# Optimization experiments

Measured on AMD Instinct MI355X. Metric: run time of the kernel, lower is better.

## Reference

```python
import jax, jax.numpy as jnp
import numpy as np

N_NODES = 65536
N_EDGES = 1048576
IN_F = 128
HID_F = 128
OUT_F = 128


def setup_inputs() -> dict:
    key = jax.random.key(0)
    ks = jax.random.split(key, 8)
    feat = jax.random.normal(ks[0], (N_NODES, IN_F), dtype=jnp.float32)
    eweight = jax.random.uniform(ks[1], (N_EDGES, 1), dtype=jnp.float32)
    W1 = jax.random.normal(ks[2], (IN_F, HID_F), dtype=jnp.float32) * (1.0 / np.sqrt(IN_F))
    b1 = jnp.zeros((HID_F,), dtype=jnp.float32)
    W2 = jax.random.normal(ks[3], (HID_F, OUT_F), dtype=jnp.float32) * (1.0 / np.sqrt(HID_F))
    b2 = jnp.zeros((OUT_F,), dtype=jnp.float32)
    src = jax.random.randint(ks[4], (N_EDGES,), 0, N_NODES, dtype=jnp.int32)
    dst = jax.random.randint(ks[5], (N_EDGES,), 0, N_NODES, dtype=jnp.int32)
    return {"feat": feat, "eweight": eweight, "W1": W1, "b1": b1,
            "W2": W2, "b2": b2, "src": src, "dst": dst}


def _degrees(src, dst, n_nodes):
    ones = jnp.ones(src.shape[0], dtype=jnp.float32)
    deg_out = jax.ops.segment_sum(ones, src, num_segments=n_nodes)
    deg_in = jax.ops.segment_sum(ones, dst, num_segments=n_nodes)
    # DGL GraphConv clamps degree to min 1 before norm='both'
    return jnp.clip(deg_out, 1.0, None), jnp.clip(deg_in, 1.0, None)


def _graph_conv(feat, W, b, src, dst, out_norm, in_norm, n_nodes):
    # DGL GraphConv, norm='both': D_out^{-1/2} x -> x W -> spmm sum -> D_in^{-1/2} -> + b
    h = feat * out_norm[:, None]
    h = h @ W
    agg = jax.ops.segment_sum(h[src], dst, num_segments=n_nodes)
    return agg * in_norm[:, None] + b


def reference(feat, eweight, W1, b1, W2, b2, src, dst):
    n = feat.shape[0]
    deg_out, deg_in = _degrees(src, dst, n)
    out_norm = jax.lax.rsqrt(deg_out)
    in_norm = jax.lax.rsqrt(deg_in)
    h = _graph_conv(feat, W1, b1, src, dst, out_norm, in_norm, n)
    h = jax.nn.relu(h)
    h = _graph_conv(h, W2, b2, src, dst, out_norm, in_norm, n)
    # final update_all: u_mul_e + sum (eweight given)
    msg = h[src] * eweight  # [E, OUT_F]
    return jax.ops.segment_sum(msg, dst, num_segments=n)
```

## Files before the change

kernel.cpp:

```cpp
#include <hip/hip_runtime.h>

#define F 128
#define NBA 512
#define NBS 128
#define COARSE 256
#define CAP_BIN 4864
#define CAP_CSR 5632

typedef unsigned int uint;
typedef unsigned short ushort;
typedef unsigned char uchar;
typedef __attribute__((ext_vector_type(8))) short short8;
typedef __attribute__((ext_vector_type(8))) unsigned short ushort8;
typedef __attribute__((ext_vector_type(4))) float floatx4;

__device__ __forceinline__ ushort f2bf(float f) {
  uint u = __float_as_uint(f);
  u += 0x7fffu + ((u >> 16) & 1u);
  return (ushort)(u >> 16);
}

__global__ __launch_bounds__(256) void w_prep(const float* __restrict__ W1,
                                              const float* __restrict__ W2,
                                              ushort* __restrict__ W1t,
                                              ushort* __restrict__ W2t,
                                              int* __restrict__ cursorD,
                                              int* __restrict__ cursorS) {
  int b = blockIdx.x;
  if (b == 0) cursorD[threadIdx.x] = 0;
  if (b == 1) cursorS[threadIdx.x] = 0;
  const float* W = (b < 64) ? W1 : W2;
  ushort* Wt = (b < 64) ? W1t : W2t;
  int idx = (b & 63) * 256 + threadIdx.x;
  int k = idx >> 7, n = idx & 127;
  Wt[n * F + k] = f2bf(W[idx]);
}

__global__ __launch_bounds__(256) void bin_edges(
    const int* __restrict__ src, const int* __restrict__ dst,
    const float* __restrict__ ew, int E,
    int* __restrict__ cursorD, int* __restrict__ cursorS,
    uint2* __restrict__ slotD, uchar* __restrict__ srcF) {
  __shared__ int cnt[4][COARSE];
  __shared__ int base[COARSE];
  bool isD = blockIdx.x < NBA;
  int blk = isD ? blockIdx.x : blockIdx.x - NBA;
  int nblk = isD ? NBA : NBS;
  const int* key = isD ? dst : src;
  int* cursor = isD ? cursorD : cursorS;
  int wave = threadIdx.x >> 6;
  for (int i = threadIdx.x; i < 4 * COARSE; i += 256) ((int*)cnt)[i] = 0;
  __syncthreads();
  int chunk = (E + nblk - 1) / nblk;
  int s0 = blk * chunk, s1 = min(E, s0 + chunk);
  for (int i = s0 + threadIdx.x; i < s1; i += 256)
    atomicAdd(&cnt[wave][key[i] >> 8], 1);
  __syncthreads();
  if (threadIdx.x < COARSE) {
    int b = threadIdx.x;
    int tot = cnt[0][b] + cnt[1][b] + cnt[2][b] + cnt[3][b];
    base[b] = tot ? atomicAdd(&cursor[b], tot) : 0;
    cnt[0][b] = 0;
  }
  __syncthreads();
  if (isD) {
    for (int i = s0 + threadIdx.x; i < s1; i += 256) {
      int d = dst[i];
      int bin = d >> 8;
      int p = base[bin] + atomicAdd(&cnt[0][bin], 1);
      if (p < CAP_BIN) {
        uint2 v;
        v.x = (uint)(src[i] & 0xffff) | ((uint)f2bf(ew[i]) << 16);
        v.y = (uint)(d & 255);
        slotD[(size_t)bin * CAP_BIN + p] = v;
      }
    }
  } else {
    for (int i = s0 + threadIdx.x; i < s1; i += 256) {
      int s = src[i];
      int bin = s >> 8;
      int p = base[bin] + atomicAdd(&cnt[0][bin], 1);
      if (p < CAP_BIN) srcF[(size_t)bin * CAP_BIN + p] = (uchar)(s & 255);
    }
  }
}

__global__ __launch_bounds__(1024) void bucket_csr(
    const uint2* __restrict__ slotD, const int* __restrict__ cursorD,
    int2* __restrict__ rowRange, float* __restrict__ inNorm, uint* __restrict__ csr,
    const uchar* __restrict__ srcF, const int* __restrict__ cursorS,
    float* __restrict__ outNorm) {
  __shared__ int hist[256], base[256], cur[256];
  int t = threadIdx.x;
  if (blockIdx.x >= COARSE) {
    int b = blockIdx.x - COARSE;
    int lo = b * CAP_BIN;
    int cntS = min(cursorS[b], CAP_BIN);
    if (t < 256) hist[t] = 0;
    __syncthreads();
    for (int i = lo + t; i < lo + cntS; i += 1024)
      atomicAdd(&hist[srcF[i]], 1);
    __syncthreads();
    if (t < 256) outNorm[b * 256 + t] = rsqrtf((float)max(hist[t], 1));
    return;
  }
  int b = blockIdx.x;
  int lo = b * CAP_BIN;
  int cntD = min(cursorD[b], CAP_BIN);
  int hi = lo + cntD;
  if (t < 256) hist[t] = 0;
  __syncthreads();
  for (int i = lo + t; i < hi; i += 1024)
    atomicAdd(&hist[slotD[i].y], 1);
  __syncthreads();
  if (t < 256) base[t] = (hist[t] + 3) & ~3;
  __syncthreads();
  for (int off = 1; off < 256; off <<= 1) {
    int x = 0;
    if (t < 256 && t >= off) x = base[t - off];
    __syncthreads();
    if (t < 256) base[t] += x;
    __syncthreads();
  }
  if (t < 256) {
    int v = hist[t];
    int sz4 = (v + 3) & ~3;
    int st = b * CAP_CSR + base[t] - sz4;
    base[t] = st;
    cur[t] = 0;
    int node = b * 256 + t;
    rowRange[node] = make_int2(st, v);
    inNorm[node] = rsqrtf((float)max(v, 1));
  }
  __syncthreads();
  for (int i = lo + t; i < hi; i += 1024) {
    uint2 v = slotD[i];
    int fine = v.y;
    int p = base[fine] + atomicAdd(&cur[fine], 1);
    csr[p] = v.x;
  }
}

template <bool BF16IN>
__global__ __launch_bounds__(256) void gemm_mfma(
    const void* __restrict__ Xv, const float* __restrict__ scale,
    const ushort* __restrict__ Wt, ushort* __restrict__ Y) {
  __shared__ ushort sA[128 * 136];
  __shared__ ushort sB[128 * 136];
  int t = threadIdx.x;
  int row0 = blockIdx.x * 128;

  {
    int r = t >> 1, hf = t & 1;
    ushort* ap = sA + r * 136 + hf * 64;
    if (BF16IN) {
      const ushort* xp = (const ushort*)Xv + (size_t)(row0 + r) * F + hf * 64;
#pragma unroll
      for (int j = 0; j < 8; ++j)
        *(ushort8*)(ap + j * 8) = *(const ushort8*)(xp + j * 8);
    } else {
      const float* xp = (const float*)Xv + (size_t)(row0 + r) * F + hf * 64;
      float s = scale[row0 + r];
#pragma unroll
      for (int j = 0; j < 8; ++j) {
        float4 v0 = *(const float4*)(xp + j * 8);
        float4 v1 = *(const float4*)(xp + j * 8 + 4);
        ushort8 o;
        o[0] = f2bf(v0.x * s); o[1] = f2bf(v0.y * s); o[2] = f2bf(v0.z * s); o[3] = f2bf(v0.w * s);
        o[4] = f2bf(v1.x * s); o[5] = f2bf(v1.y * s); o[6] = f2bf(v1.z * s); o[7] = f2bf(v1.w * s);
        *(ushort8*)(ap + j * 8) = o;
      }
    }
  }
  {
    int n = t >> 1, hf = t & 1;
    const ushort* wp = Wt + n * F + hf * 64;
    ushort* bp = sB + n * 136 + hf * 64;
#pragma unroll
    for (int j = 0; j < 8; ++j)
      *(ushort8*)(bp + j * 8) = *(const ushort8*)(wp + j * 8);
  }
  __syncthreads();

  int lane = t & 63, wave = t >> 6;
  int quad = lane >> 4, l16 = lane & 15;
  int mrow0 = wave * 32;

  floatx4 acc[2][8];
#pragma unroll
  for (int a = 0; a < 2; ++a)
#pragma unroll
    for (int c = 0; c < 8; ++c) acc[a][c] = (floatx4){0.f, 0.f, 0.f, 0.f};

#pragma unroll
  for (int kc = 0; kc < 128; kc += 32) {
    short8 afrag[2], bfrag[8];
#pragma unroll
    for (int a = 0; a < 2; ++a)
      afrag[a] = *(const short8*)(sA + (mrow0 + a * 16 + l16) * 136 + kc + quad * 8);
#pragma unroll
    for (int c = 0; c < 8; ++c)
      bfrag[c] = *(const short8*)(sB + (c * 16 + l16) * 136 + kc + quad * 8);
#pragma unroll
    for (int a = 0; a < 2; ++a)
#pragma unroll
      for (int c = 0; c < 8; ++c)
        acc[a][c] = __builtin_amdgcn_mfma_f32_16x16x32_bf16(afrag[a], bfrag[c], acc[a][c], 0, 0, 0);
  }

#pragma unroll
  for (int a = 0; a < 2; ++a)
#pragma unroll
    for (int c = 0; c < 8; ++c)
#pragma unroll
      for (int r = 0; r < 4; ++r) {
        int row = row0 + mrow0 + a * 16 + quad * 4 + r;
        int col = c * 16 + l16;
        Y[(size_t)row * F + col] = f2bf(acc[a][c][r]);
      }
}


template <bool EW, bool NB, bool RELU, bool PS, bool OUT_BF16>
__global__ __launch_bounds__(256) void spmm(
    const ushort* __restrict__ hb, const int2* __restrict__ rowRange,
    const uint* __restrict__ csr, const float* __restrict__ inNorm,
    const float* __restrict__ bias, const float* __restrict__ postScale,
    void* __restrict__ outv) {
  int wave = threadIdx.x >> 6;
  int lane = threadIdx.x & 63;
  int n0 = blockIdx.x * 8 + wave * 2;
  int n1 = n0 + 1;
  int2 rA = rowRange[n0];
  int2 rB = rowRange[n1];

#define EDGE(e, X, Y)                                                          \
  {                                                                            \
    uint w = *((const uint*)(hb + ((size_t)((e) & 0xffffu) << 7)) + lane);     \
    float q = EW ? __uint_as_float((e) & 0xffff0000u) : 1.f;                   \
    X = fmaf(__uint_as_float(w << 16), q, X);                                  \
    Y = fmaf(__uint_as_float(w & 0xffff0000u), q, Y);                          \
  }
#define DO4(c, X, Y) \
  EDGE((c).x, X[0], Y[0]) EDGE((c).y, X[1], Y[1]) EDGE((c).z, X[2], Y[2]) EDGE((c).w, X[3], Y[3])

  float AX[4] = {0.f, 0.f, 0.f, 0.f}, AY[4] = {0.f, 0.f, 0.f, 0.f};
  float BX[4] = {0.f, 0.f, 0.f, 0.f}, BY[4] = {0.f, 0.f, 0.f, 0.f};
  int iA = 0, iB = 0;
  int lA = rA.y, lB = rB.y;

  while (iA + 8 <= lA && iB + 8 <= lB) {
    uint4 a0 = *(const uint4*)(csr + rA.x + iA);
    uint4 a1 = *(const uint4*)(csr + rA.x + iA + 4);
    uint4 b0 = *(const uint4*)(csr + rB.x + iB);
    uint4 b1 = *(const uint4*)(csr + rB.x + iB + 4);
    DO4(a0, AX, AY) DO4(a1, AX, AY) DO4(b0, BX, BY) DO4(b1, BX, BY)
    iA += 8; iB += 8;
  }
  while (iA + 8 <= lA) {
    uint4 a0 = *(const uint4*)(csr + rA.x + iA);
    uint4 a1 = *(const uint4*)(csr + rA.x + iA + 4);
    DO4(a0, AX, AY) DO4(a1, AX, AY)
    iA += 8;
  }
  if (iA + 4 <= lA) {
    uint4 a0 = *(const uint4*)(csr + rA.x + iA);
    DO4(a0, AX, AY)
    iA += 4;
  }
  if (iA < lA) {
    uint4 c = *(const uint4*)(csr + rA.x + iA);
    uint ee[4] = {c.x, c.y, c.z, c.w};
    int r = lA - iA;
#pragma unroll
    for (int j = 0; j < 3; ++j)
      if (j < r) EDGE(ee[j], AX[j], AY[j])
  }
  while (iB + 8 <= lB) {
    uint4 b0 = *(const uint4*)(csr + rB.x + iB);
    uint4 b1 = *(const uint4*)(csr + rB.x + iB + 4);
    DO4(b0, BX, BY) DO4(b1, BX, BY)
    iB += 8;
  }
  if (iB + 4 <= lB) {
    uint4 b0 = *(const uint4*)(csr + rB.x + iB);
    DO4(b0, BX, BY)
    iB += 4;
  }
  if (iB < lB) {
    uint4 c = *(const uint4*)(csr + rB.x + iB);
    uint ee[4] = {c.x, c.y, c.z, c.w};
    int r = lB - iB;
#pragma unroll
    for (int j = 0; j < 3; ++j)
      if (j < r) EDGE(ee[j], BX[j], BY[j])
  }
#undef DO4
#undef EDGE

  float rxA = (AX[0] + AX[1]) + (AX[2] + AX[3]);
  float ryA = (AY[0] + AY[1]) + (AY[2] + AY[3]);
  float rxB = (BX[0] + BX[1]) + (BX[2] + BX[3]);
  float ryB = (BY[0] + BY[1]) + (BY[2] + BY[3]);
  if (NB) {
    float2 bv = *((const float2*)bias + lane);
    float scA = inNorm[n0], scB = inNorm[n1];
    rxA = fmaf(rxA, scA, bv.x); ryA = fmaf(ryA, scA, bv.y);
    rxB = fmaf(rxB, scB, bv.x); ryB = fmaf(ryB, scB, bv.y);
    if (RELU) {
      rxA = fmaxf(rxA, 0.f); ryA = fmaxf(ryA, 0.f);
      rxB = fmaxf(rxB, 0.f); ryB = fmaxf(ryB, 0.f);
    }
    if (PS) {
      float oA = postScale[n0], oB = postScale[n1];
      rxA *= oA; ryA *= oA; rxB *= oB; ryB *= oB;
    }
  }
  if (OUT_BF16) {
    uint pA = ((uint)f2bf(ryA) << 16) | (uint)f2bf(rxA);
    uint pB = ((uint)f2bf(ryB) << 16) | (uint)f2bf(rxB);
    *((uint*)outv + ((size_t)n0 << 6) + lane) = pA;
    *((uint*)outv + ((size_t)n1 << 6) + lane) = pB;
  } else {
    float2 vA = {rxA, ryA};
    float2 vB = {rxB, ryB};
    *((float2*)outv + ((size_t)n0 << 6) + lane) = vA;
    *((float2*)outv + ((size_t)n1 << 6) + lane) = vB;
  }
}


extern "C" void kernel_launch(void* const* d_in, const int* in_sizes, int n_in,
                              void* d_out, int out_size, void* d_ws, size_t ws_size,
                              hipStream_t stream) {
  const float* feat = (const float*)d_in[0];
  const float* ew   = (const float*)d_in[1];
  const float* W1   = (const float*)d_in[2];
  const float* b1   = (const float*)d_in[3];
  const float* W2   = (const float*)d_in[4];
  const float* b2   = (const float*)d_in[5];
  const int*   src  = (const int*)d_in[6];
  const int*   dst  = (const int*)d_in[7];
  const int N = in_sizes[0] / F;
  const int E = in_sizes[6];
  float* out = (float*)d_out;

  char* ws = (char*)d_ws;
  size_t off = 0;
  auto alloc = [&](size_t bytes) {
    void* p = ws + off;
    off += (bytes + 255) & ~(size_t)255;
    return p;
  };
  int2*   rowRange = (int2*)alloc((size_t)N * 8);
  float*  inNorm   = (float*)alloc((size_t)N * 4);
  float*  outNorm  = (float*)alloc((size_t)N * 4);
  ushort* W1t      = (ushort*)alloc((size_t)F * F * 2);
  ushort* W2t      = (ushort*)alloc((size_t)F * F * 2);
  int*    cursorD  = (int*)alloc(COARSE * 4);
  int*    cursorS  = (int*)alloc(COARSE * 4);
  uint*   csr      = (uint*)alloc((size_t)COARSE * CAP_CSR * 4);
  ushort* bufAb    = (ushort*)alloc((size_t)N * F * 2);
  ushort* bufBb    = (ushort*)alloc((size_t)N * F * 2);
  ushort* bufCb    = (ushort*)alloc((size_t)N * F * 2);
  if (off > ws_size) return;

  uint2* slotD;
  uchar* srcF;
  {
    char* tp = (char*)bufBb;
    size_t toff = 0;
    auto talloc = [&](size_t bytes) {
      void* p = tp + toff;
      toff += (bytes + 255) & ~(size_t)255;
      return p;
    };
    slotD = (uint2*)talloc((size_t)COARSE * CAP_BIN * 8);
    srcF  = (uchar*)talloc((size_t)COARSE * CAP_BIN);
  }

  w_prep<<<128, 256, 0, stream>>>(W1, W2, W1t, W2t, cursorD, cursorS);
  bin_edges<<<NBA + NBS, 256, 0, stream>>>(src, dst, ew, E, cursorD, cursorS, slotD, srcF);
  bucket_csr<<<2 * COARSE, 1024, 0, stream>>>(slotD, cursorD, rowRange, inNorm, csr,
                                              srcF, cursorS, outNorm);

  gemm_mfma<false><<<N / 128, 256, 0, stream>>>(feat, outNorm, W1t, bufAb);
  spmm<false, true, true, true, true><<<N / 8, 256, 0, stream>>>(
      bufAb, rowRange, csr, inNorm, b1, outNorm, bufBb);
  gemm_mfma<true><<<N / 128, 256, 0, stream>>>(bufBb, nullptr, W2t, bufAb);
  spmm<false, true, false, false, true><<<N / 8, 256, 0, stream>>>(
      bufAb, rowRange, csr, inNorm, b2, nullptr, bufCb);
  spmm<true, false, false, false, false><<<N / 8, 256, 0, stream>>>(
      bufCb, rowRange, csr, nullptr, nullptr, nullptr, out);
}
```

Measured before the change: 277.5 us.

## Split each wave across four edge groups with 16-byte row gathers in SpMM

```diff
diff --git a/kernel.cpp b/kernel.cpp
--- a/kernel.cpp
+++ b/kernel.cpp
@@ -131,6 +131,7 @@
     int node = b * 256 + t;
     rowRange[node] = make_int2(st, v);
     inNorm[node] = rsqrtf((float)max(v, 1));
+    for (int p = st + v; p < st + sz4; ++p) csr[p] = 0x80000000u;
   }
   __syncthreads();
   for (int i = lo + t; i < hi; i += 1024) {
@@ -227,105 +228,96 @@
     const uint* __restrict__ csr, const float* __restrict__ inNorm,
     const float* __restrict__ bias, const float* __restrict__ postScale,
     void* __restrict__ outv) {
-  int wave = threadIdx.x >> 6;
   int lane = threadIdx.x & 63;
-  int n0 = blockIdx.x * 8 + wave * 2;
-  int n1 = n0 + 1;
-  int2 rA = rowRange[n0];
-  int2 rB = rowRange[n1];
-
-#define EDGE(e, X, Y)                                                          \
-  {                                                                            \
-    uint w = *((const uint*)(hb + ((size_t)((e) & 0xffffu) << 7)) + lane);     \
-    float q = EW ? __uint_as_float((e) & 0xffff0000u) : 1.f;                   \
-    X = fmaf(__uint_as_float(w << 16), q, X);                                  \
-    Y = fmaf(__uint_as_float(w & 0xffff0000u), q, Y);                          \
-  }
-#define DO4(c, X, Y) \
-  EDGE((c).x, X[0], Y[0]) EDGE((c).y, X[1], Y[1]) EDGE((c).z, X[2], Y[2]) EDGE((c).w, X[3], Y[3])
-
-  float AX[4] = {0.f, 0.f, 0.f, 0.f}, AY[4] = {0.f, 0.f, 0.f, 0.f};
-  float BX[4] = {0.f, 0.f, 0.f, 0.f}, BY[4] = {0.f, 0.f, 0.f, 0.f};
-  int iA = 0, iB = 0;
-  int lA = rA.y, lB = rB.y;
-
-  while (iA + 8 <= lA && iB + 8 <= lB) {
-    uint4 a0 = *(const uint4*)(csr + rA.x + iA);
-    uint4 a1 = *(const uint4*)(csr + rA.x + iA + 4);
-    uint4 b0 = *(const uint4*)(csr + rB.x + iB);
-    uint4 b1 = *(const uint4*)(csr + rB.x + iB + 4);
-    DO4(a0, AX, AY) DO4(a1, AX, AY) DO4(b0, BX, BY) DO4(b1, BX, BY)
-    iA += 8; iB += 8;
-  }
-  while (iA + 8 <= lA) {
-    uint4 a0 = *(const uint4*)(csr + rA.x + iA);
-    uint4 a1 = *(const uint4*)(csr + rA.x + iA + 4);
-    DO4(a0, AX, AY) DO4(a1, AX, AY)
-    iA += 8;
-  }
-  if (iA + 4 <= lA) {
-    uint4 a0 = *(const uint4*)(csr + rA.x + iA);
-    DO4(a0, AX, AY)
-    iA += 4;
-  }
-  if (iA < lA) {
-    uint4 c = *(const uint4*)(csr + rA.x + iA);
-    uint ee[4] = {c.x, c.y, c.z, c.w};
-    int r = lA - iA;
-#pragma unroll
-    for (int j = 0; j < 3; ++j)
-      if (j < r) EDGE(ee[j], AX[j], AY[j])
-  }
-  while (iB + 8 <= lB) {
-    uint4 b0 = *(const uint4*)(csr + rB.x + iB);
-    uint4 b1 = *(const uint4*)(csr + rB.x + iB + 4);
-    DO4(b0, BX, BY) DO4(b1, BX, BY)
-    iB += 8;
-  }
-  if (iB + 4 <= lB) {
-    uint4 b0 = *(const uint4*)(csr + rB.x + iB);
-    DO4(b0, BX, BY)
-    iB += 4;
-  }
-  if (iB < lB) {
-    uint4 c = *(const uint4*)(csr + rB.x + iB);
-    uint ee[4] = {c.x, c.y, c.z, c.w};
-    int r = lB - iB;
-#pragma unroll
-    for (int j = 0; j < 3; ++j)
-      if (j < r) EDGE(ee[j], BX[j], BY[j])
-  }
-#undef DO4
-#undef EDGE
-
-  float rxA = (AX[0] + AX[1]) + (AX[2] + AX[3]);
-  float ryA = (AY[0] + AY[1]) + (AY[2] + AY[3]);
-  float rxB = (BX[0] + BX[1]) + (BX[2] + BX[3]);
-  float ryB = (BY[0] + BY[1]) + (BY[2] + BY[3]);
+  int g = lane >> 4;
+  int j = lane & 15;
+  int n = blockIdx.x * 4 + (threadIdx.x >> 6);
+  int2 r = rowRange[n];
+  int len4 = (r.y + 3) & ~3;
+  const char* hbB = (const char*)hb;
+  uint joff = (uint)j << 4;
+  float acc[8] = {0.f, 0.f, 0.f, 0.f, 0.f, 0.f, 0.f, 0.f};
+
+#define GQ(e, c, q)                                                      \
+  {                                                                      \
+    uint ei = (e);                                                       \
+    c = *(const uint4*)(hbB + (((ei & 0xffffu) << 8) | joff));           \
+    q = EW ? __uint_as_float(ei & 0xffff0000u)                           \
+           : ((int)ei >= 0 ? 1.0f : 0.0f);                               \
+  }
+#define ACC8(c, q)                                                      \
+  {                                                                     \
+    acc[0] = fmaf(__uint_as_float(c.x << 16), q, acc[0]);               \
+    acc[1] = fmaf(__uint_as_float(c.x & 0xffff0000u), q, acc[1]);       \
+    acc[2] = fmaf(__uint_as_float(c.y << 16), q, acc[2]);               \
+    acc[3] = fmaf(__uint_as_float(c.y & 0xffff0000u), q, acc[3]);       \
+    acc[4] = fmaf(__uint_as_float(c.z << 16), q, acc[4]);               \
+    acc[5] = fmaf(__uint_as_float(c.z & 0xffff0000u), q, acc[5]);       \
+    acc[6] = fmaf(__uint_as_float(c.w << 16), q, acc[6]);               \
+    acc[7] = fmaf(__uint_as_float(c.w & 0xffff0000u), q, acc[7]);       \
+  }
+
+  int i = 0;
+  for (; i + 16 <= len4; i += 16) {
+    uint4 ee = *(const uint4*)(csr + r.x + i + 4 * g);
+    uint4 c0, c1, c2, c3;
+    float q0, q1, q2, q3;
+    GQ(ee.x, c0, q0) GQ(ee.y, c1, q1) GQ(ee.z, c2, q2) GQ(ee.w, c3, q3)
+    ACC8(c0, q0) ACC8(c1, q1) ACC8(c2, q2) ACC8(c3, q3)
+  }
+  if (i + 8 <= len4) {
+    uint2 ee = *(const uint2*)(csr + r.x + i + 2 * g);
+    uint4 c0, c1;
+    float q0, q1;
+    GQ(ee.x, c0, q0) GQ(ee.y, c1, q1)
+    ACC8(c0, q0) ACC8(c1, q1)
+    i += 8;
+  }
+  if (i < len4) {
+    uint e = csr[r.x + i + g];
+    uint4 c0;
+    float q0;
+    GQ(e, c0, q0)
+    ACC8(c0, q0)
+  }
+#undef GQ
+#undef ACC8
+
+#pragma unroll
+  for (int k = 0; k < 8; ++k) {
+    acc[k] += __shfl_xor(acc[k], 16, 64);
+    acc[k] += __shfl_xor(acc[k], 32, 64);
+  }
+  if (g != 0) return;
+
   if (NB) {
-    float2 bv = *((const float2*)bias + lane);
-    float scA = inNorm[n0], scB = inNorm[n1];
-    rxA = fmaf(rxA, scA, bv.x); ryA = fmaf(ryA, scA, bv.y);
-    rxB = fmaf(rxB, scB, bv.x); ryB = fmaf(ryB, scB, bv.y);
-    if (RELU) {
-      rxA = fmaxf(rxA, 0.f); ryA = fmaxf(ryA, 0.f);
-      rxB = fmaxf(rxB, 0.f); ryB = fmaxf(ryB, 0.f);
+    float sc = inNorm[n];
+    float4 b0 = ((const float4*)bias)[2 * j];
+    float4 b1 = ((const float4*)bias)[2 * j + 1];
+    float bb[8] = {b0.x, b0.y, b0.z, b0.w, b1.x, b1.y, b1.z, b1.w};
+#pragma unroll
+    for (int k = 0; k < 8; ++k) {
+      acc[k] = fmaf(acc[k], sc, bb[k]);
+      if (RELU) acc[k] = fmaxf(acc[k], 0.f);
     }
     if (PS) {
-      float oA = postScale[n0], oB = postScale[n1];
-      rxA *= oA; ryA *= oA; rxB *= oB; ryB *= oB;
+      float o = postScale[n];
+#pragma unroll
+      for (int k = 0; k < 8; ++k) acc[k] *= o;
     }
   }
   if (OUT_BF16) {
-    uint pA = ((uint)f2bf(ryA) << 16) | (uint)f2bf(rxA);
-    uint pB = ((uint)f2bf(ryB) << 16) | (uint)f2bf(rxB);
-    *((uint*)outv + ((size_t)n0 << 6) + lane) = pA;
-    *((uint*)outv + ((size_t)n1 << 6) + lane) = pB;
+    uint4 o;
+    o.x = ((uint)f2bf(acc[1]) << 16) | (uint)f2bf(acc[0]);
+    o.y = ((uint)f2bf(acc[3]) << 16) | (uint)f2bf(acc[2]);
+    o.z = ((uint)f2bf(acc[5]) << 16) | (uint)f2bf(acc[4]);
+    o.w = ((uint)f2bf(acc[7]) << 16) | (uint)f2bf(acc[6]);
+    ((uint4*)outv)[(size_t)n * 16 + j] = o;
   } else {
-    float2 vA = {rxA, ryA};
-    float2 vB = {rxB, ryB};
-    *((float2*)outv + ((size_t)n0 << 6) + lane) = vA;
-    *((float2*)outv + ((size_t)n1 << 6) + lane) = vB;
+    float4 lo = {acc[0], acc[1], acc[2], acc[3]};
+    float4 hi = {acc[4], acc[5], acc[6], acc[7]};
+    ((float4*)outv)[(size_t)n * 32 + 2 * j] = lo;
+    ((float4*)outv)[(size_t)n * 32 + 2 * j + 1] = hi;
   }
 }
 
@@ -385,11 +377,11 @@
                                               srcF, cursorS, outNorm);
 
   gemm_mfma<false><<<N / 128, 256, 0, stream>>>(feat, outNorm, W1t, bufAb);
-  spmm<false, true, true, true, true><<<N / 8, 256, 0, stream>>>(
+  spmm<false, true, true, true, true><<<N / 4, 256, 0, stream>>>(
       bufAb, rowRange, csr, inNorm, b1, outNorm, bufBb);
   gemm_mfma<true><<<N / 128, 256, 0, stream>>>(bufBb, nullptr, W2t, bufAb);
-  spmm<false, true, false, false, true><<<N / 8, 256, 0, stream>>>(
+  spmm<false, true, false, false, true><<<N / 4, 256, 0, stream>>>(
       bufAb, rowRange, csr, inNorm, b2, nullptr, bufCb);
-  spmm<true, false, false, false, false><<<N / 8, 256, 0, stream>>>(
+  spmm<true, false, false, false, false><<<N / 4, 256, 0, stream>>>(
       bufCb, rowRange, csr, nullptr, nullptr, nullptr, out);
 }
```

Result: no change. 273.8 us (-1.3%).
